# Kernel optimization log

Hardware: AMD Instinct MI355X
Metric: run time of the kernel (lower is better)

Reference implementation:

```python
import jax, jax.numpy as jnp
import numpy as np

GROUP_SIZE = 128


def setup_inputs() -> dict:
    key = jax.random.key(0)
    k1, k2, k3 = jax.random.split(key, 3)
    B, S, IN, OUT = 4, 8192, 1024, 1024
    x = jax.random.normal(k1, (B, S, IN), dtype=jnp.float32)
    weight = jax.random.normal(k2, (OUT, IN), dtype=jnp.float32) * 0.02
    bias = jax.random.normal(k3, (OUT,), dtype=jnp.float32) * 0.01
    return {"x": x, "weight": weight, "bias": bias}


def reference(x, weight, bias):
    """Quantized int8 path: quantize() + _forward_int8 of OneBitLinear.

    - weights binarized to +/-1 int8 (sign, with 0 -> -1, matching
      sign().clamp(min=0) bit packing then 2*bit-1)
    - per-group weight scales = group absmax, stored fp16 (as in quantize())
    - activations dynamically quantized per-token to int8
    - int32-accumulated GEMM, rescaled by x_scale * mean group scale per row
    """
    out_f, in_f = weight.shape
    ng = in_f // GROUP_SIZE
    w_g = weight.reshape(out_f, ng, GROUP_SIZE)
    # per-group absmax scales, cast fp16 -> fp32 to mimic fp16 storage
    scales = jnp.maximum(jnp.max(jnp.abs(w_g), axis=-1), 1e-8)
    scales = scales.astype(jnp.float16).astype(jnp.float32)  # [O, ng]
    # +/-1 int8 weights (sign>0 -> +1, else -1; zero maps to -1 like the packer)
    w_int8 = jnp.where(weight > 0, 1, -1).astype(jnp.int8)  # [O, I]

    # dynamic per-token activation quantization
    x_f = x.reshape(-1, in_f)  # [BT, I]
    x_scale = jnp.maximum(jnp.max(jnp.abs(x_f), axis=1, keepdims=True), 1e-8) / 127.0
    x_int8 = jnp.clip(jnp.round(x_f / x_scale), -128, 127).astype(jnp.int8)

    # int8 GEMM with int32 accumulation
    out_i32 = jnp.matmul(
        x_int8.astype(jnp.int32), w_int8.T.astype(jnp.int32)
    )  # [BT, O]

    w_scale_per_row = jnp.mean(scales, axis=1)  # [O]
    out_f32 = out_i32.astype(jnp.float32) * x_scale * w_scale_per_row[None, :]
    out_f32 = out_f32 + bias[None, :]
    return out_f32.reshape(*x.shape[:-1], out_f)
```

## Files before the change

### kernel.cpp

```cpp
#include <hip/hip_runtime.h>
#include <hip/hip_fp16.h>

#define K_DIM 1024
#define N_DIM 1024

typedef int v4i __attribute__((ext_vector_type(4)));

__device__ __forceinline__ void async_load16(const void* g, void* l) {
    __builtin_amdgcn_global_load_lds(
        (const __attribute__((address_space(1))) unsigned int*)g,
        (__attribute__((address_space(3))) unsigned int*)l,
        16, 0, 0);
}

__global__ __launch_bounds__(256) void prep_w(const float* __restrict__ w,
                                              signed char* __restrict__ wq,
                                              float* __restrict__ wscale) {
    const int lane = threadIdx.x & 63;
    const int row  = blockIdx.x * 4 + (threadIdx.x >> 6);
    const float4* wr = (const float4*)(w + (size_t)row * K_DIM);
    float4 v[4];
#pragma unroll
    for (int j = 0; j < 4; ++j) v[j] = wr[lane * 4 + j];

    float g = 0.f;
#pragma unroll
    for (int j = 0; j < 4; ++j) {
        g = fmaxf(g, fabsf(v[j].x)); g = fmaxf(g, fabsf(v[j].y));
        g = fmaxf(g, fabsf(v[j].z)); g = fmaxf(g, fabsf(v[j].w));
    }
    g = fmaxf(g, __shfl_xor(g, 1, 64));
    g = fmaxf(g, __shfl_xor(g, 2, 64));
    g = fmaxf(g, __shfl_xor(g, 4, 64));
    const float s = __half2float(__float2half(fmaxf(g, 1e-8f)));
    float t = s;
    t += __shfl_xor(t, 8, 64);
    t += __shfl_xor(t, 16, 64);
    t += __shfl_xor(t, 32, 64);
    if (lane == 0) wscale[row] = t * 0.125f;

    int pk[4];
#pragma unroll
    for (int j = 0; j < 4; ++j) {
        const int b0 = (v[j].x > 0.f) ? 1 : -1;
        const int b1 = (v[j].y > 0.f) ? 1 : -1;
        const int b2 = (v[j].z > 0.f) ? 1 : -1;
        const int b3 = (v[j].w > 0.f) ? 1 : -1;
        pk[j] = (b0 & 255) | ((b1 & 255) << 8) | ((b2 & 255) << 16) | (b3 << 24);
    }
    *(int4*)(wq + (size_t)row * K_DIM + lane * 16) = make_int4(pk[0], pk[1], pk[2], pk[3]);
}

__global__ __launch_bounds__(256) void quant_x(const float* __restrict__ x,
                                               signed char* __restrict__ xq,
                                               float* __restrict__ xs) {
    const int lane = threadIdx.x & 63;
    const int row  = blockIdx.x * 4 + (threadIdx.x >> 6);
    const float4* xr = (const float4*)(x + (size_t)row * K_DIM);
    float4 v[4];
#pragma unroll
    for (int j = 0; j < 4; ++j) v[j] = xr[lane * 4 + j];

    float am = 0.f;
#pragma unroll
    for (int j = 0; j < 4; ++j) {
        am = fmaxf(am, fabsf(v[j].x)); am = fmaxf(am, fabsf(v[j].y));
        am = fmaxf(am, fabsf(v[j].z)); am = fmaxf(am, fabsf(v[j].w));
    }
#pragma unroll
    for (int off = 32; off >= 1; off >>= 1) am = fmaxf(am, __shfl_xor(am, off, 64));
    const float scale = fmaxf(am, 1e-8f) / 127.f;
    const float inv   = 1.0f / scale;

    int pk[4];
#pragma unroll
    for (int j = 0; j < 4; ++j) {
        const int b0 = (int)fminf(fmaxf(rintf(v[j].x * inv), -128.f), 127.f);
        const int b1 = (int)fminf(fmaxf(rintf(v[j].y * inv), -128.f), 127.f);
        const int b2 = (int)fminf(fmaxf(rintf(v[j].z * inv), -128.f), 127.f);
        const int b3 = (int)fminf(fmaxf(rintf(v[j].w * inv), -128.f), 127.f);
        pk[j] = (b0 & 255) | ((b1 & 255) << 8) | ((b2 & 255) << 16) | (b3 << 24);
    }
    *(int4*)(xq + (size_t)row * K_DIM + lane * 16) = make_int4(pk[0], pk[1], pk[2], pk[3]);
    if (lane == 0) xs[row] = scale;
}

__global__ __launch_bounds__(256) void gemm_i8(const signed char* __restrict__ A,
                                               const signed char* __restrict__ Bw,
                                               const float* __restrict__ xs,
                                               const float* __restrict__ wscale,
                                               const float* __restrict__ bias,
                                               float* __restrict__ out) {
    __shared__ __align__(16) signed char As[128 * 128];
    __shared__ __align__(16) signed char Bs[128 * 128];

    const int tid  = threadIdx.x;
    const int lane = tid & 63;
    const int wave = tid >> 6;
    const int wm = wave >> 1;
    const int wn = wave & 1;

    const int bid = blockIdx.x;
    const int xcd = bid & 7;
    const int q   = bid >> 3;
    const int mT  = xcd * 32 + (q >> 3);
    const int nT  = q & 7;
    const size_t mBase = (size_t)mT * 128;
    const int    nBase = nT * 128;

    v4i acc[4][4] = {};

    const int srow = tid >> 3;
    const int scol = (((tid & 7) ^ (srow & 7))) * 16;
    const signed char* Ag = A  + (mBase + srow) * K_DIM + scol;
    const signed char* Bg = Bw + (size_t)(nBase + srow) * K_DIM + scol;

    for (int kt = 0; kt < 8; ++kt) {
        const int koff = kt * 128;
#pragma unroll
        for (int c = 0; c < 4; ++c) {
            async_load16(Ag + (size_t)(c * 32) * K_DIM + koff, As + c * 4096 + tid * 16);
            async_load16(Bg + (size_t)(c * 32) * K_DIM + koff, Bs + c * 4096 + tid * 16);
        }
        __syncthreads();

        const int r16 = lane & 15;
        const int g   = lane >> 4;
        const int x7  = lane & 7;
#pragma unroll
        for (int ks = 0; ks < 2; ++ks) {
            const int co = ((ks * 4 + g) ^ x7) * 16;
            v4i af[4], bf[4];
#pragma unroll
            for (int mt = 0; mt < 4; ++mt)
                af[mt] = *(const v4i*)(As + (wm * 64 + mt * 16 + r16) * 128 + co);
#pragma unroll
            for (int nt = 0; nt < 4; ++nt)
                bf[nt] = *(const v4i*)(Bs + (wn * 64 + nt * 16 + r16) * 128 + co);
#pragma unroll
            for (int mt = 0; mt < 4; ++mt)
#pragma unroll
                for (int nt = 0; nt < 4; ++nt)
                    acc[mt][nt] = __builtin_amdgcn_mfma_i32_16x16x64_i8(
                        af[mt], bf[nt], acc[mt][nt], 0, 0, 0);
        }
        __syncthreads();
    }

    const int cc = lane & 15;
    const int rq = (lane >> 4) * 4;
    float xsr[4][4];
#pragma unroll
    for (int mt = 0; mt < 4; ++mt)
#pragma unroll
        for (int i = 0; i < 4; ++i)
            xsr[mt][i] = xs[mBase + wm * 64 + mt * 16 + rq + i];

#pragma unroll
    for (int nt = 0; nt < 4; ++nt) {
        const int col  = nBase + wn * 64 + nt * 16 + cc;
        const float wsc = wscale[col];
        const float bb  = bias[col];
#pragma unroll
        for (int mt = 0; mt < 4; ++mt) {
#pragma unroll
            for (int i = 0; i < 4; ++i) {
                const size_t row = mBase + wm * 64 + mt * 16 + rq + i;
                out[row * N_DIM + col] = ((float)acc[mt][nt][i] * xsr[mt][i]) * wsc + bb;
            }
        }
    }
}

extern "C" void kernel_launch(void* const* d_in, const int* in_sizes, int n_in,
                              void* d_out, int out_size, void* d_ws, size_t ws_size,
                              hipStream_t stream) {
    const float* x    = (const float*)d_in[0];
    const float* w    = (const float*)d_in[1];
    const float* bias = (const float*)d_in[2];
    float* out = (float*)d_out;

    const int BT = in_sizes[0] / K_DIM;

    char* ws = (char*)d_ws;
    signed char* xq     = (signed char*)ws;
    float*       xs     = (float*)(ws + (size_t)BT * K_DIM);
    signed char* wq     = (signed char*)(ws + (size_t)BT * K_DIM + (size_t)BT * 4);
    float*       wscale = (float*)((char*)wq + (size_t)N_DIM * K_DIM);

    prep_w<<<N_DIM / 4, 256, 0, stream>>>(w, wq, wscale);
    quant_x<<<BT / 4, 256, 0, stream>>>(x, xq, xs);
    gemm_i8<<<(BT / 128) * (N_DIM / 128), 256, 0, stream>>>(xq, wq, xs, wscale, bias, out);
}
```

Before: 276.6 us.

## Fuse activation quantization into GEMM with register-resident A and streamed weights

Removes the separate quant_x kernel: each block quantizes its 128 full-K rows of x directly into a 128KB LDS buffer, then keeps the whole A slice in registers and loops over all 8 N tiles, streaming weight chunks through a double-buffered LDS ring with async loads. This avoids the int8 activation round-trip to global memory and the repeated A reloads across N tiles. In exchange it launches only BT/128 = 256 blocks at one block per CU, each doing serial quantization up front, and issues a barrier per 64-wide K step, so latency hiding and occupancy drop.

```diff
diff --git a/kernel.cpp b/kernel.cpp
--- a/kernel.cpp
+++ b/kernel.cpp
@@ -51,123 +51,123 @@
     *(int4*)(wq + (size_t)row * K_DIM + lane * 16) = make_int4(pk[0], pk[1], pk[2], pk[3]);
 }
 
-__global__ __launch_bounds__(256) void quant_x(const float* __restrict__ x,
-                                               signed char* __restrict__ xq,
-                                               float* __restrict__ xs) {
-    const int lane = threadIdx.x & 63;
-    const int row  = blockIdx.x * 4 + (threadIdx.x >> 6);
-    const float4* xr = (const float4*)(x + (size_t)row * K_DIM);
-    float4 v[4];
-#pragma unroll
-    for (int j = 0; j < 4; ++j) v[j] = xr[lane * 4 + j];
-
-    float am = 0.f;
-#pragma unroll
-    for (int j = 0; j < 4; ++j) {
-        am = fmaxf(am, fabsf(v[j].x)); am = fmaxf(am, fabsf(v[j].y));
-        am = fmaxf(am, fabsf(v[j].z)); am = fmaxf(am, fabsf(v[j].w));
-    }
-#pragma unroll
-    for (int off = 32; off >= 1; off >>= 1) am = fmaxf(am, __shfl_xor(am, off, 64));
-    const float scale = fmaxf(am, 1e-8f) / 127.f;
-    const float inv   = 1.0f / scale;
-
-    int pk[4];
-#pragma unroll
-    for (int j = 0; j < 4; ++j) {
-        const int b0 = (int)fminf(fmaxf(rintf(v[j].x * inv), -128.f), 127.f);
-        const int b1 = (int)fminf(fmaxf(rintf(v[j].y * inv), -128.f), 127.f);
-        const int b2 = (int)fminf(fmaxf(rintf(v[j].z * inv), -128.f), 127.f);
-        const int b3 = (int)fminf(fmaxf(rintf(v[j].w * inv), -128.f), 127.f);
-        pk[j] = (b0 & 255) | ((b1 & 255) << 8) | ((b2 & 255) << 16) | (b3 << 24);
-    }
-    *(int4*)(xq + (size_t)row * K_DIM + lane * 16) = make_int4(pk[0], pk[1], pk[2], pk[3]);
-    if (lane == 0) xs[row] = scale;
-}
-
-__global__ __launch_bounds__(256) void gemm_i8(const signed char* __restrict__ A,
-                                               const signed char* __restrict__ Bw,
-                                               const float* __restrict__ xs,
-                                               const float* __restrict__ wscale,
-                                               const float* __restrict__ bias,
-                                               float* __restrict__ out) {
-    __shared__ __align__(16) signed char As[128 * 128];
-    __shared__ __align__(16) signed char Bs[128 * 128];
+__global__ __launch_bounds__(256, 1) void fused_qgemm(
+        const float* __restrict__ x,
+        const signed char* __restrict__ wq,
+        const float* __restrict__ wscale,
+        const float* __restrict__ bias,
+        float* __restrict__ out) {
+    __shared__ __align__(16) signed char As[128 * 1024];
+    __shared__ __align__(16) signed char Bsm[2][128 * 64];
+    __shared__ float xsL[128];
 
     const int tid  = threadIdx.x;
     const int lane = tid & 63;
     const int wave = tid >> 6;
-    const int wm = wave >> 1;
-    const int wn = wave & 1;
+    const int wm = wave >> 1, wn = wave & 1;
+    const size_t mBase = (size_t)blockIdx.x * 128;
 
-    const int bid = blockIdx.x;
-    const int xcd = bid & 7;
-    const int q   = bid >> 3;
-    const int mT  = xcd * 32 + (q >> 3);
-    const int nT  = q & 7;
-    const size_t mBase = (size_t)mT * 128;
-    const int    nBase = nT * 128;
+    for (int r = 0; r < 32; ++r) {
+        const int row = wave * 32 + r;
+        const float4* xr = (const float4*)(x + (mBase + row) * K_DIM);
+        float4 v[4];
+#pragma unroll
+        for (int j = 0; j < 4; ++j) v[j] = xr[lane * 4 + j];
+        float am = 0.f;
+#pragma unroll
+        for (int j = 0; j < 4; ++j) {
+            am = fmaxf(am, fabsf(v[j].x)); am = fmaxf(am, fabsf(v[j].y));
+            am = fmaxf(am, fabsf(v[j].z)); am = fmaxf(am, fabsf(v[j].w));
+        }
+#pragma unroll
+        for (int off = 32; off >= 1; off >>= 1) am = fmaxf(am, __shfl_xor(am, off, 64));
+        const float scale = fmaxf(am, 1e-8f) / 127.f;
+        const float inv   = 1.0f / scale;
+        int pk[4];
+#pragma unroll
+        for (int j = 0; j < 4; ++j) {
+            const int b0 = (int)fminf(fmaxf(rintf(v[j].x * inv), -128.f), 127.f);
+            const int b1 = (int)fminf(fmaxf(rintf(v[j].y * inv), -128.f), 127.f);
+            const int b2 = (int)fminf(fmaxf(rintf(v[j].z * inv), -128.f), 127.f);
+            const int b3 = (int)fminf(fmaxf(rintf(v[j].w * inv), -128.f), 127.f);
+            pk[j] = (b0 & 255) | ((b1 & 255) << 8) | ((b2 & 255) << 16) | (b3 << 24);
+        }
+        *(int4*)(As + row * 1024 + ((lane ^ (row & 7)) << 4)) =
+            make_int4(pk[0], pk[1], pk[2], pk[3]);
+        if (lane == 0) xsL[row] = scale;
+    }
+    __syncthreads();
 
-    v4i acc[4][4] = {};
-
-    const int srow = tid >> 3;
-    const int scol = (((tid & 7) ^ (srow & 7))) * 16;
-    const signed char* Ag = A  + (mBase + srow) * K_DIM + scol;
-    const signed char* Bg = Bw + (size_t)(nBase + srow) * K_DIM + scol;
-
-    for (int kt = 0; kt < 8; ++kt) {
-        const int koff = kt * 128;
+    const int r16 = lane & 15, g = lane >> 4, x7 = lane & 7;
+    v4i areg[4][16];
 #pragma unroll
-        for (int c = 0; c < 4; ++c) {
-            async_load16(Ag + (size_t)(c * 32) * K_DIM + koff, As + c * 4096 + tid * 16);
-            async_load16(Bg + (size_t)(c * 32) * K_DIM + koff, Bs + c * 4096 + tid * 16);
-        }
-        __syncthreads();
-
-        const int r16 = lane & 15;
-        const int g   = lane >> 4;
-        const int x7  = lane & 7;
+    for (int mt = 0; mt < 4; ++mt) {
+        const signed char* Ab = As + (wm * 64 + mt * 16 + r16) * 1024;
 #pragma unroll
-        for (int ks = 0; ks < 2; ++ks) {
-            const int co = ((ks * 4 + g) ^ x7) * 16;
-            v4i af[4], bf[4];
-#pragma unroll
-            for (int mt = 0; mt < 4; ++mt)
-                af[mt] = *(const v4i*)(As + (wm * 64 + mt * 16 + r16) * 128 + co);
-#pragma unroll
-            for (int nt = 0; nt < 4; ++nt)
-                bf[nt] = *(const v4i*)(Bs + (wn * 64 + nt * 16 + r16) * 128 + co);
-#pragma unroll
-            for (int mt = 0; mt < 4; ++mt)
-#pragma unroll
-                for (int nt = 0; nt < 4; ++nt)
-                    acc[mt][nt] = __builtin_amdgcn_mfma_i32_16x16x64_i8(
-                        af[mt], bf[nt], acc[mt][nt], 0, 0, 0);
-        }
-        __syncthreads();
+        for (int s = 0; s < 16; ++s)
+            areg[mt][s] = *(const v4i*)(Ab + (((s * 4 + g) ^ x7) << 4));
     }
-
-    const int cc = lane & 15;
-    const int rq = (lane >> 4) * 4;
+    const int rq = g * 4;
     float xsr[4][4];
 #pragma unroll
     for (int mt = 0; mt < 4; ++mt)
 #pragma unroll
         for (int i = 0; i < 4; ++i)
-            xsr[mt][i] = xs[mBase + wm * 64 + mt * 16 + rq + i];
+            xsr[mt][i] = xsL[wm * 64 + mt * 16 + rq + i];
 
+    const size_t bOff = (size_t)(tid >> 2) * K_DIM + (((tid & 3) ^ ((tid >> 3) & 3)) << 4);
+    int bfo[4];
 #pragma unroll
-    for (int nt = 0; nt < 4; ++nt) {
-        const int col  = nBase + wn * 64 + nt * 16 + cc;
-        const float wsc = wscale[col];
-        const float bb  = bias[col];
+    for (int nt4 = 0; nt4 < 4; ++nt4) {
+        const int rowb = wn * 64 + nt4 * 16 + r16;
+        bfo[nt4] = rowb * 64 + ((g ^ ((rowb >> 1) & 3)) << 4);
+    }
+
+    {
+        const signed char* src = wq + bOff;
+        async_load16(src,         Bsm[0] + tid * 16);
+        async_load16(src + 65536, Bsm[0] + 4096 + tid * 16);
+    }
+    __syncthreads();
+
+    const int cc = lane & 15;
+    for (int nt = 0; nt < 8; ++nt) {
+        v4i acc[4][4] = {};
 #pragma unroll
-        for (int mt = 0; mt < 4; ++mt) {
+        for (int s = 0; s < 16; ++s) {
+            const int S = nt * 16 + s;
+            if (S < 127) {
+                const int Sn = S + 1;
+                const signed char* src = wq + (size_t)(Sn >> 4) * (128 * K_DIM)
+                                            + (size_t)(Sn & 15) * 64 + bOff;
+                signed char* dst = Bsm[Sn & 1] + tid * 16;
+                async_load16(src,         dst);
+                async_load16(src + 65536, dst + 4096);
+            }
+            const signed char* bb = Bsm[s & 1];
+            v4i bf[4];
 #pragma unroll
-            for (int i = 0; i < 4; ++i) {
-                const size_t row = mBase + wm * 64 + mt * 16 + rq + i;
-                out[row * N_DIM + col] = ((float)acc[mt][nt][i] * xsr[mt][i]) * wsc + bb;
-            }
+            for (int nt4 = 0; nt4 < 4; ++nt4)
+                bf[nt4] = *(const v4i*)(bb + bfo[nt4]);
+#pragma unroll
+            for (int mt = 0; mt < 4; ++mt)
+#pragma unroll
+                for (int nt4 = 0; nt4 < 4; ++nt4)
+                    acc[mt][nt4] = __builtin_amdgcn_mfma_i32_16x16x64_i8(
+                        areg[mt][s], bf[nt4], acc[mt][nt4], 0, 0, 0);
+            __syncthreads();
+        }
+#pragma unroll
+        for (int nt4 = 0; nt4 < 4; ++nt4) {
+            const int col  = nt * 128 + wn * 64 + nt4 * 16 + cc;
+            const float wsc = wscale[col];
+            const float bbv = bias[col];
+#pragma unroll
+            for (int mt = 0; mt < 4; ++mt)
+#pragma unroll
+                for (int i = 0; i < 4; ++i)
+                    out[(mBase + wm * 64 + mt * 16 + rq + i) * N_DIM + col] =
+                        (float)acc[mt][nt4][i] * xsr[mt][i] * wsc + bbv;
         }
     }
 }
@@ -183,12 +183,9 @@
     const int BT = in_sizes[0] / K_DIM;
 
     char* ws = (char*)d_ws;
-    signed char* xq     = (signed char*)ws;
-    float*       xs     = (float*)(ws + (size_t)BT * K_DIM);
-    signed char* wq     = (signed char*)(ws + (size_t)BT * K_DIM + (size_t)BT * 4);
-    float*       wscale = (float*)((char*)wq + (size_t)N_DIM * K_DIM);
+    signed char* wq     = (signed char*)ws;
+    float*       wscale = (float*)(ws + (size_t)N_DIM * K_DIM);
 
     prep_w<<<N_DIM / 4, 256, 0, stream>>>(w, wq, wscale);
-    quant_x<<<BT / 4, 256, 0, stream>>>(x, xq, xs);
-    gemm_i8<<<(BT / 128) * (N_DIM / 128), 256, 0, stream>>>(xq, wq, xs, wscale, bias, out);
+    fused_qgemm<<<BT / 128, 256, 0, stream>>>(x, wq, wscale, bias, out);
 }
```

Result: slower. 336.5 us (+21.6%).
